# Performance work log

Hardware: AMD Instinct MI355X
Metric: run time of the kernel (lower is better)

## Reference

```python
import jax, jax.numpy as jnp
from jax import lax
import numpy as np

H = 128          # hidden_dim
VOCAB = 200000   # word_dim
L = 32           # words per node
NUM_LEAVES = 2048
NUM_PARENTS = 2047
MAXC = 4         # max child slots in a tree row
NCLASS = 4


def setup_inputs() -> dict:
    key = jax.random.key(0)
    ks = jax.random.split(key, 16)
    N = NUM_LEAVES + NUM_PARENTS
    x_word = jax.random.uniform(ks[0], (N, L), dtype=jnp.float32)
    x_index = jax.random.randint(ks[1], (N, L), 0, VOCAB)
    # caterpillar tree: parent idx has one leaf child and the previous parent
    idx = np.arange(NUM_PARENTS)
    tree = np.full((NUM_PARENTS, MAXC), -1, dtype=np.int32)
    tree[:, 0] = idx
    tree[:, 1] = np.where(idx > 0, NUM_LEAVES + idx - 1, NUM_LEAVES - 1)
    tree = jnp.asarray(tree)
    y = jax.random.uniform(ks[2], (NCLASS,), dtype=jnp.float32)
    def init(k, shp):
        return 0.1 * jax.random.normal(k, shp, dtype=jnp.float32)
    return dict(
        x_word=x_word, x_index=x_index, tree=tree, y=y,
        E_bu=init(ks[3], (H, VOCAB)),
        WQ=init(ks[4], (H, H)), WK=init(ks[5], (H, H)), WV=init(ks[6], (H, H)),
        W_z=init(ks[7], (H, H)), U_z=init(ks[8], (H, H)), b_z=jnp.zeros((H,), jnp.float32),
        W_r=init(ks[9], (H, H)), U_r=init(ks[10], (H, H)), b_r=jnp.zeros((H,), jnp.float32),
        W_h=init(ks[11], (H, H)), U_h=init(ks[12], (H, H)), b_h=jnp.zeros((H,), jnp.float32),
        W_out=init(ks[13], (NCLASS, H)), b_out=jnp.zeros((NCLASS,), jnp.float32),
    )


def _forward(x_word, y, E_bu, WQ, WK, WV, W_z, U_z, b_z, W_r, U_r, b_r,
             W_h, U_h, b_h, W_out, b_out, x_index, tree):
    Hd = E_bu.shape[0]
    # parent_xe for every node: weighted sum of embedding columns  [N, H]
    emb = E_bu.T[x_index]                        # [N, L, H] gather
    xe = jnp.einsum('nlh,nl->nh', emb, x_word)
    n_parents = tree.shape[0]
    n_leaves = x_word.shape[0] - n_parents

    def cell(xe_i, h_tilde):
        # W.mul(v).sum(dim=1) == W @ v in the torch code
        z = jax.nn.sigmoid(W_z @ xe_i + U_z @ h_tilde + b_z)
        r = jax.nn.sigmoid(W_r @ xe_i + U_r @ h_tilde + b_r)
        c = jnp.tanh(W_h @ xe_i + U_h @ (h_tilde * r) + b_h)
        return z * h_tilde + (1.0 - z) * c

    # leaves: child_h == 0  =>  h_tilde == 0 (vectorized over all leaves)
    xe_leaf = xe[:n_leaves]
    z_l = jax.nn.sigmoid(xe_leaf @ W_z.T + b_z)
    c_l = jnp.tanh(xe_leaf @ W_h.T + b_h)
    leaf_h = (1.0 - z_l) * c_l

    node_h0 = jnp.zeros((x_word.shape[0], Hd), xe.dtype).at[:n_leaves].set(leaf_h)
    scale = 1.0 / jnp.sqrt(jnp.asarray(Hd, xe.dtype))

    def step(node_h, inp):
        xe_p, row, i = inp
        mask = row >= 0
        child_h = node_h[jnp.clip(row, 0)]                  # [MAXC, H]
        query = jax.nn.sigmoid(xe_p @ WQ)                   # sigmoid(xe @ WQ)
        keyv = child_h @ WK
        val = child_h @ WV
        scores = jnp.where(mask, (query * scale * keyv).sum(-1), -1e9)
        attn = jax.nn.softmax(scores)                       # over children
        h_tilde = attn @ val
        h = cell(xe_p, h_tilde)
        return node_h.at[i].set(h), h

    idxs = jnp.arange(n_parents) + n_leaves
    _, parent_hs = lax.scan(step, node_h0, (xe[n_leaves:], tree, idxs))
    root = parent_hs[-1]
    pred = jax.nn.softmax(W_out @ root + b_out)
    loss = jnp.sum((y - pred) ** 2)
    return pred, loss


def reference(x_word, x_index, tree, y, E_bu, WQ, WK, WV, W_z, U_z, b_z,
              W_r, U_r, b_r, W_h, U_h, b_h, W_out, b_out):
    return _forward(x_word, y, E_bu, WQ, WK, WV, W_z, U_z, b_z, W_r, U_r, b_r,
                    W_h, U_h, b_h, W_out, b_out, x_index, tree)
```

## Files before the change

kernel.cpp:

```cpp
#include <hip/hip_runtime.h>
#include <math.h>

#define HD 128
#define LW 32
#define VOCABN 200000
#define NLEAF 2048
#define NPAR 2047
#define NNODE 4095
#define MAXC 4
#define NCLASS 4
#define SCALE 0.08838834764831845f

#define OFF_XE   0
#define OFF_NODE 524160
#define OFF_W3   786304
#define OFF_WQ   851840
#define OFF_AZ   1113856
#define OFF_AR   1375872
#define OFF_AH   1637888
#define OFF_PREV 1899904
#define OFF_ES   2685952
#define OFF_HG   2688000
#define OFF_HTR  2688128
#define OFF_ET   2688256
#define WS_END   (OFF_ET + (size_t)VOCABN * HD)

#define BARL() asm volatile("s_waitcnt lgkmcnt(0)\n\ts_barrier" ::: "memory")
#define PIN4(v) asm volatile("" : "+v"((v).x), "+v"((v).y), "+v"((v).z), "+v"((v).w))
#define LD4(p, k) (*(const float4*)((p) + 4 * (k)))

typedef __attribute__((ext_vector_type(16))) float fx16;

#define CH(W, X, n4) { a0 += (W).x * (X)[4*(n4)+0] + (W).y * (X)[4*(n4)+1]; \
                       a1 += (W).z * (X)[4*(n4)+2] + (W).w * (X)[4*(n4)+3]; }

__global__ void k_xe(const float* __restrict__ xw, const int* __restrict__ xi,
                     const float* __restrict__ E, float* __restrict__ xe) {
    int n = blockIdx.x;
    int h = threadIdx.x;
    __shared__ int   sidx[LW];
    __shared__ float sw[LW];
    if (h < LW) { sidx[h] = xi[n * LW + h]; sw[h] = xw[n * LW + h]; }
    __syncthreads();
    float acc = 0.f;
#pragma unroll
    for (int l = 0; l < LW; ++l)
        acc += E[(size_t)h * VOCABN + sidx[l]] * sw[l];
    xe[(size_t)n * HD + h] = acc;
}

__global__ void k_transpose(const float* __restrict__ E, float* __restrict__ ET) {
    __shared__ float tile[32][33];
    int vb = blockIdx.x * 32, hb = blockIdx.y * 32;
    int tx = threadIdx.x, ty = threadIdx.y;
#pragma unroll
    for (int r = 0; r < 32; r += 8)
        tile[ty + r][tx] = E[(size_t)(hb + ty + r) * VOCABN + vb + tx];
    __syncthreads();
#pragma unroll
    for (int r = 0; r < 32; r += 8)
        ET[(size_t)(vb + ty + r) * HD + hb + tx] = tile[tx][ty + r];
}

__global__ void k_xe_t(const float* __restrict__ xw, const int* __restrict__ xi,
                       const float* __restrict__ ET, float* __restrict__ xe) {
    int n = blockIdx.x;
    int h = threadIdx.x;
    __shared__ int   sidx[LW];
    __shared__ float sw[LW];
    if (h < LW) { sidx[h] = xi[n * LW + h]; sw[h] = xw[n * LW + h]; }
    __syncthreads();
    float acc = 0.f;
#pragma unroll
    for (int l = 0; l < LW; ++l)
        acc += ET[(size_t)sidx[l] * HD + h] * sw[l];
    xe[(size_t)n * HD + h] = acc;
}

__global__ void k_leaf(const float* __restrict__ xe, const float* __restrict__ Wz,
                       const float* __restrict__ bz, const float* __restrict__ Wh,
                       const float* __restrict__ bh, float* __restrict__ node_h) {
    int n = blockIdx.x;
    int j = threadIdx.x;
    __shared__ float xl[HD];
    xl[j] = xe[(size_t)n * HD + j];
    __syncthreads();
    float az = bz[j], ah = bh[j];
    const float* wzr = Wz + (size_t)j * HD;
    const float* whr = Wh + (size_t)j * HD;
#pragma unroll 4
    for (int k = 0; k < HD; ++k) { az += wzr[k] * xl[k]; ah += whr[k] * xl[k]; }
    float z = 1.f / (1.f + expf(-az));
    float c = tanhf(ah);
    node_h[(size_t)n * HD + j] = (1.f - z) * c;
}

__global__ void k_fuse(const float* __restrict__ WV, const float* __restrict__ Uz,
                       const float* __restrict__ Ur, const float* __restrict__ Uh,
                       float* __restrict__ w3) {
    int r = blockIdx.x;
    int b = threadIdx.x;
    float v;
    if (r < 128) {
        v = WV[(size_t)b * HD + r];
    } else if (r < 384) {
        const float* u  = (r < 256 ? Uz + (size_t)(r - 128) * HD : Ur + (size_t)(r - 256) * HD);
        const float* wv = WV + (size_t)b * HD;
        float a = 0.f;
#pragma unroll 4
        for (int j = 0; j < HD; ++j) a += u[j] * wv[j];
        v = a;
    } else {
        v = Uh[(size_t)(r - 384) * HD + b];
    }
    w3[(size_t)r * HD + b] = v;
}

__global__ void k_ppre(const float* __restrict__ xe, const float* __restrict__ WQ,
                       const float* __restrict__ WK, const float* __restrict__ Wz,
                       const float* __restrict__ bz, const float* __restrict__ Wr,
                       const float* __restrict__ br, const float* __restrict__ Wh,
                       const float* __restrict__ bh, float* __restrict__ wq,
                       float* __restrict__ az, float* __restrict__ ar,
                       float* __restrict__ ah) {
    int i = blockIdx.x;
    int j = threadIdx.x;
    __shared__ float xl[HD], ql[HD];
    xl[j] = xe[(size_t)(NLEAF + i) * HD + j];
    __syncthreads();
    float q = 0.f;
#pragma unroll 4
    for (int h = 0; h < HD; ++h) q += xl[h] * WQ[(size_t)h * HD + j];
    ql[j] = 1.f / (1.f + expf(-q));
    __syncthreads();
    float w = 0.f;
#pragma unroll 4
    for (int k = 0; k < HD; ++k) w += WK[(size_t)j * HD + k] * ql[k];
    wq[(size_t)i * HD + j] = w;
    float vz = bz[j], vr = br[j], vh = bh[j];
#pragma unroll 4
    for (int k = 0; k < HD; ++k) {
        float xv = xl[k];
        vz += Wz[(size_t)j * HD + k] * xv;
        vr += Wr[(size_t)j * HD + k] * xv;
        vh += Wh[(size_t)j * HD + k] * xv;
    }
    az[(size_t)i * HD + j] = vz;
    ar[(size_t)i * HD + j] = vr;
    ah[(size_t)i * HD + j] = vh;
}

__global__ void k_chpre(const int* __restrict__ tree, const float* __restrict__ node_h,
                        const float* __restrict__ w3, const float* __restrict__ wq_all,
                        float* __restrict__ preVexp, float* __restrict__ expsum) {
    int i = blockIdx.x;
    int j = threadIdx.x;
    __shared__ float hl[HD];
    __shared__ float red[HD];
    float wqj = wq_all[(size_t)i * HD + j];
    float acc0 = 0.f, acc1 = 0.f, acc2 = 0.f, esum = 0.f;
    for (int c = 0; c < MAXC; ++c) {
        int child = tree[i * MAXC + c];
        if (child < 0 || child >= NLEAF) continue;
        __syncthreads();
        hl[j] = node_h[(size_t)child * HD + j];
        __syncthreads();
        red[j] = hl[j] * wqj;
        __syncthreads();
        for (int s = 64; s > 0; s >>= 1) {
            if (j < s) red[j] += red[j + s];
            __syncthreads();
        }
        float e = expf(red[0] * SCALE);
        float d0 = 0.f, d1 = 0.f, d2 = 0.f;
#pragma unroll 4
        for (int k = 0; k < HD; ++k) {
            float x = hl[k];
            d0 += w3[(size_t)j * HD + k] * x;
            d1 += w3[(size_t)(128 + j) * HD + k] * x;
            d2 += w3[(size_t)(256 + j) * HD + k] * x;
        }
        acc0 += e * d0; acc1 += e * d1; acc2 += e * d2; esum += e;
    }
    preVexp[(size_t)i * 384 + j]       = acc0;
    preVexp[(size_t)i * 384 + 128 + j] = acc1;
    preVexp[(size_t)i * 384 + 256 + j] = acc2;
    if (j == 0) expsum[i] = esum;
}

__global__ __launch_bounds__(768, 3) void k_seq(
    float* __restrict__ ws, const float* __restrict__ Wout,
    const float* __restrict__ bout, const float* __restrict__ y,
    float* __restrict__ out) {
    const float* w3      = ws + OFF_W3;
    const float* wq_all  = ws + OFF_WQ;
    const float* az_all  = ws + OFF_AZ;
    const float* ar_all  = ws + OFF_AR;
    const float* ah_all  = ws + OFF_AH;
    const float* preVexp = ws + OFF_PREV;
    const float* expsum  = ws + OFF_ES;
    float* h_glob   = ws + OFF_HG;
    float* htr_glob = ws + OFF_HTR;

    const int t   = threadIdx.x;
    const int l   = t & 63;
    const int w   = t >> 6;
    const int q   = w & 1;
    const int row = 64 * (w >> 1) + l;
    const int w8  = w & 7;
    const int kq  = w8 & 3;
    const int row3 = 64 * (w8 >> 2) + l;

    __shared__ float part1[768];
    __shared__ __align__(16) float part3[HD][4];
    __shared__ float sPart[2];
    __shared__ float h_lds[HD];
    __shared__ float outv[NCLASS];

    const float* wp = w3 + (size_t)row * HD + 64 * q;
    float4 A0 = LD4(wp, 0),  A1 = LD4(wp, 1),  A2 = LD4(wp, 2),  A3 = LD4(wp, 3),
           A4 = LD4(wp, 4),  A5 = LD4(wp, 5),  A6 = LD4(wp, 6),  A7 = LD4(wp, 7),
           A8 = LD4(wp, 8),  A9 = LD4(wp, 9),  A10 = LD4(wp, 10), A11 = LD4(wp, 11),
           A12 = LD4(wp, 12), A13 = LD4(wp, 13), A14 = LD4(wp, 14), A15 = LD4(wp, 15);
    const float* wp3 = w3 + (size_t)(384 + row3) * HD + 32 * kq;
    float4 B0 = LD4(wp3, 0), B1 = LD4(wp3, 1), B2 = LD4(wp3, 2), B3 = LD4(wp3, 3),
           B4 = LD4(wp3, 4), B5 = LD4(wp3, 5), B6 = LD4(wp3, 6), B7 = LD4(wp3, 7);
    PIN4(A0); PIN4(A1); PIN4(A2); PIN4(A3); PIN4(A4); PIN4(A5); PIN4(A6); PIN4(A7);
    PIN4(A8); PIN4(A9); PIN4(A10); PIN4(A11); PIN4(A12); PIN4(A13); PIN4(A14); PIN4(A15);
    PIN4(B0); PIN4(B1); PIN4(B2); PIN4(B3); PIN4(B4); PIN4(B5); PIN4(B6); PIN4(B7);

    const float* xp1 = h_glob + __builtin_amdgcn_readfirstlane(64 * q);
    const float* xp3 = htr_glob + __builtin_amdgcn_readfirstlane(32 * kq);

    float pv0 = 0.f, pv1 = 0.f, pv2 = 0.f, paz = 0.f, par = 0.f, pah = 0.f,
          pwq = 0.f, pes = 0.f;
    if (t < HD) {
        pv0 = preVexp[t];       pv1 = preVexp[128 + t]; pv2 = preVexp[256 + t];
        paz = az_all[t];        par = ar_all[t];        pah = ah_all[t];
        pwq = wq_all[(size_t)HD + t];
        pes = expsum[0];
        h_glob[t] = 0.f;
    }
    if (t < 2) sPart[t] = (t == 0) ? -1e30f : 0.f;
    asm volatile("s_waitcnt vmcnt(0)" ::: "memory");
    __syncthreads();

    float zreg = 0.f, htreg = 0.f, hfin = 0.f;

    for (int i = 0; i < NPAR; ++i) {
        const int inext = (i + 1 < NPAR) ? i + 1 : NPAR - 1;
        const int in2   = (i + 2 < NPAR) ? i + 2 : NPAR - 1;

        {
            fx16 x0, x1, x2, x3;
            asm volatile(
                "s_dcache_inv\n\t"
                "s_load_dwordx16 %0, %4, 0x0\n\t"
                "s_load_dwordx16 %1, %4, 0x40\n\t"
                "s_load_dwordx16 %2, %4, 0x80\n\t"
                "s_load_dwordx16 %3, %4, 0xC0\n\t"
                "s_waitcnt lgkmcnt(0)"
                : "=s"(x0), "=s"(x1), "=s"(x2), "=s"(x3)
                : "s"(xp1));
            float a0 = 0.f, a1 = 0.f;
            CH(A0, x0, 0)  CH(A1, x0, 1)  CH(A2, x0, 2)  CH(A3, x0, 3)
            CH(A4, x1, 0)  CH(A5, x1, 1)  CH(A6, x1, 2)  CH(A7, x1, 3)
            CH(A8, x2, 0)  CH(A9, x2, 1)  CH(A10, x2, 2) CH(A11, x2, 3)
            CH(A12, x3, 0) CH(A13, x3, 1) CH(A14, x3, 2) CH(A15, x3, 3)
            part1[q * 384 + row] = a0 + a1;
        }
        BARL();

        if (t < HD) {
            float vdot = part1[t]       + part1[384 + t];
            float zdot = part1[128 + t] + part1[384 + 128 + t];
            float rdot = part1[256 + t] + part1[384 + 256 + t];
            float sc   = sPart[0] + sPart[1];
            float e    = expf(sc);
            float inv  = 1.f / (pes + e);
            float htv  = (pv0 + e * vdot) * inv;
            float z    = 1.f / (1.f + expf(-(paz + (pv1 + e * zdot) * inv)));
            float rr   = 1.f / (1.f + expf(-(par + (pv2 + e * rdot) * inv)));
            htr_glob[t] = htv * rr;
            zreg = z; htreg = htv;
            asm volatile("s_waitcnt vmcnt(0)" ::: "memory");
        }
        BARL();

        if (w < 8) {
            fx16 x0, x1;
            asm volatile(
                "s_dcache_inv\n\t"
                "s_load_dwordx16 %0, %2, 0x0\n\t"
                "s_load_dwordx16 %1, %2, 0x40\n\t"
                "s_waitcnt lgkmcnt(0)"
                : "=s"(x0), "=s"(x1)
                : "s"(xp3));
            float a0 = 0.f, a1 = 0.f;
            CH(B0, x0, 0) CH(B1, x0, 1) CH(B2, x0, 2) CH(B3, x0, 3)
            CH(B4, x1, 0) CH(B5, x1, 1) CH(B6, x1, 2) CH(B7, x1, 3)
            part3[row3][kq] = a0 + a1;
        }
        BARL();

        if (t < HD) {
            float4 p3 = *(const float4*)part3[t];
            float u   = (p3.x + p3.y) + (p3.z + p3.w);
            float c   = tanhf(pah + u);
            float hv  = zreg * htreg + (1.f - zreg) * c;
            hfin = hv;
            h_glob[t] = hv;
            pv0 = preVexp[(size_t)inext * 384 + t];
            pv1 = preVexp[(size_t)inext * 384 + 128 + t];
            pv2 = preVexp[(size_t)inext * 384 + 256 + t];
            paz = az_all[(size_t)inext * HD + t];
            par = ar_all[(size_t)inext * HD + t];
            pah = ah_all[(size_t)inext * HD + t];
            pes = expsum[inext];
            float prod = hv * pwq;
#pragma unroll
            for (int o = 32; o > 0; o >>= 1) prod += __shfl_down(prod, o, 64);
            if (l == 0) sPart[t >> 6] = prod * SCALE;
            pwq = wq_all[(size_t)in2 * HD + t];
            asm volatile("s_waitcnt vmcnt(0)" ::: "memory");
        }
        BARL();
    }

    if (t < HD) h_lds[t] = hfin;
    __syncthreads();
    if (t < NCLASS) {
        float acc = bout[t];
#pragma unroll 4
        for (int k = 0; k < HD; ++k) acc += Wout[(size_t)t * HD + k] * h_lds[k];
        outv[t] = acc;
    }
    __syncthreads();
    if (t == 0) {
        float m  = fmaxf(fmaxf(outv[0], outv[1]), fmaxf(outv[2], outv[3]));
        float e0 = expf(outv[0] - m), e1 = expf(outv[1] - m);
        float e2 = expf(outv[2] - m), e3 = expf(outv[3] - m);
        float inv = 1.f / (e0 + e1 + e2 + e3);
        float p0 = e0 * inv, p1 = e1 * inv, p2 = e2 * inv, p3 = e3 * inv;
        out[0] = p0; out[1] = p1; out[2] = p2; out[3] = p3;
        float d0 = y[0] - p0, d1 = y[1] - p1, d2 = y[2] - p2, d3 = y[3] - p3;
        out[4] = d0 * d0 + d1 * d1 + d2 * d2 + d3 * d3;
    }
}

extern "C" void kernel_launch(void* const* d_in, const int* in_sizes, int n_in,
                              void* d_out, int out_size, void* d_ws, size_t ws_size,
                              hipStream_t stream) {
    const float* x_word  = (const float*)d_in[0];
    const int*   x_index = (const int*)d_in[1];
    const int*   tree    = (const int*)d_in[2];
    const float* y       = (const float*)d_in[3];
    const float* E_bu    = (const float*)d_in[4];
    const float* WQ      = (const float*)d_in[5];
    const float* WK      = (const float*)d_in[6];
    const float* WV      = (const float*)d_in[7];
    const float* W_z     = (const float*)d_in[8];
    const float* U_z     = (const float*)d_in[9];
    const float* b_z     = (const float*)d_in[10];
    const float* W_r     = (const float*)d_in[11];
    const float* U_r     = (const float*)d_in[12];
    const float* b_r     = (const float*)d_in[13];
    const float* W_h     = (const float*)d_in[14];
    const float* U_h     = (const float*)d_in[15];
    const float* b_h     = (const float*)d_in[16];
    const float* W_out   = (const float*)d_in[17];
    const float* b_out   = (const float*)d_in[18];

    float* ws      = (float*)d_ws;
    float* xe      = ws + OFF_XE;
    float* node_h  = ws + OFF_NODE;
    float* w3      = ws + OFF_W3;
    float* wq      = ws + OFF_WQ;
    float* az      = ws + OFF_AZ;
    float* ar      = ws + OFF_AR;
    float* ah      = ws + OFF_AH;
    float* preVexp = ws + OFF_PREV;
    float* expsum  = ws + OFF_ES;
    float* ET      = ws + OFF_ET;

    bool use_transpose = ws_size >= WS_END * sizeof(float);

    if (use_transpose) {
        dim3 tg(VOCABN / 32, HD / 32), tb(32, 8);
        k_transpose<<<tg, tb, 0, stream>>>(E_bu, ET);
        k_xe_t<<<NNODE, HD, 0, stream>>>(x_word, x_index, ET, xe);
    } else {
        k_xe<<<NNODE, HD, 0, stream>>>(x_word, x_index, E_bu, xe);
    }
    k_leaf<<<NLEAF, HD, 0, stream>>>(xe, W_z, b_z, W_h, b_h, node_h);
    k_fuse<<<512, HD, 0, stream>>>(WV, U_z, U_r, U_h, w3);
    k_ppre<<<NPAR, HD, 0, stream>>>(xe, WQ, WK, W_z, b_z, W_r, b_r, W_h, b_h,
                                    wq, az, ar, ah);
    k_chpre<<<NPAR, HD, 0, stream>>>(tree, node_h, w3, wq, preVexp, expsum);
    k_seq<<<1, 768, 0, stream>>>(ws, W_out, b_out, y, (float*)d_out);
}
```

Before: 4.415 ms.

## Split sequential GRU phases onto dedicated waves in 1024-thread block

The single-block sequential kernel grows from 768 to 1024 threads. Waves 0-11 hold the V/Z/R recurrent weights and waves 12-15 hold the U_h weights, each as 64 registers, so no wave keeps two weight sets and the second matvec is split two ways instead of four. The prefetch of the next step's precomputed terms moves from the last phase into the second phase so it overlaps the U_h matvec. More waves per block raise register pressure under the 4-waves-per-EU limit and add extra waves at every barrier.

```diff
diff --git a/kernel.cpp b/kernel.cpp
--- a/kernel.cpp
+++ b/kernel.cpp
@@ -33,6 +33,10 @@
 
 #define CH(W, X, n4) { a0 += (W).x * (X)[4*(n4)+0] + (W).y * (X)[4*(n4)+1]; \
                        a1 += (W).z * (X)[4*(n4)+2] + (W).w * (X)[4*(n4)+3]; }
+
+#define PIN_ALL() do { PIN4(A0); PIN4(A1); PIN4(A2); PIN4(A3); \
+    PIN4(A4); PIN4(A5); PIN4(A6); PIN4(A7); PIN4(A8); PIN4(A9); \
+    PIN4(A10); PIN4(A11); PIN4(A12); PIN4(A13); PIN4(A14); PIN4(A15); } while (0)
 
 __global__ void k_xe(const float* __restrict__ xw, const int* __restrict__ xi,
                      const float* __restrict__ E, float* __restrict__ xe) {
@@ -188,70 +192,63 @@
     if (j == 0) expsum[i] = esum;
 }
 
-__global__ __launch_bounds__(768, 3) void k_seq(
-    float* __restrict__ ws, const float* __restrict__ Wout,
-    const float* __restrict__ bout, const float* __restrict__ y,
-    float* __restrict__ out) {
-    const float* w3      = ws + OFF_W3;
-    const float* wq_all  = ws + OFF_WQ;
-    const float* az_all  = ws + OFF_AZ;
-    const float* ar_all  = ws + OFF_AR;
-    const float* ah_all  = ws + OFF_AH;
-    const float* preVexp = ws + OFF_PREV;
-    const float* expsum  = ws + OFF_ES;
-    float* h_glob   = ws + OFF_HG;
-    float* htr_glob = ws + OFF_HTR;
-
-    const int t   = threadIdx.x;
-    const int l   = t & 63;
-    const int w   = t >> 6;
-    const int q   = w & 1;
-    const int row = 64 * (w >> 1) + l;
-    const int w8  = w & 7;
-    const int kq  = w8 & 3;
-    const int row3 = 64 * (w8 >> 2) + l;
+__global__ __launch_bounds__(1024)
+__attribute__((amdgpu_waves_per_eu(4, 4)))
+void k_seq(float* __restrict__ ws, const float* __restrict__ Wout,
+           const float* __restrict__ bout, const float* __restrict__ y,
+           float* __restrict__ out) {
+    const int t  = threadIdx.x;
+    const int l  = t & 63;
+    const int w  = t >> 6;
+    const bool isP1 = (w < 12);
+    const int q1   = w & 1;
+    const int row1 = 64 * (w >> 1) + l;
+    const int w12  = w - 12;
+    const int q3   = w12 & 1;
+    const int row3 = 64 * (w12 >> 1) + l;
 
     __shared__ float part1[768];
-    __shared__ __align__(16) float part3[HD][4];
+    __shared__ float part3[256];
     __shared__ float sPart[2];
     __shared__ float h_lds[HD];
     __shared__ float outv[NCLASS];
 
-    const float* wp = w3 + (size_t)row * HD + 64 * q;
+    const int woff = isP1 ? (row1 * HD + 64 * q1)
+                          : ((384 + row3) * HD + 64 * q3);
+    const float* wp = ws + OFF_W3 + woff;
     float4 A0 = LD4(wp, 0),  A1 = LD4(wp, 1),  A2 = LD4(wp, 2),  A3 = LD4(wp, 3),
            A4 = LD4(wp, 4),  A5 = LD4(wp, 5),  A6 = LD4(wp, 6),  A7 = LD4(wp, 7),
            A8 = LD4(wp, 8),  A9 = LD4(wp, 9),  A10 = LD4(wp, 10), A11 = LD4(wp, 11),
            A12 = LD4(wp, 12), A13 = LD4(wp, 13), A14 = LD4(wp, 14), A15 = LD4(wp, 15);
-    const float* wp3 = w3 + (size_t)(384 + row3) * HD + 32 * kq;
-    float4 B0 = LD4(wp3, 0), B1 = LD4(wp3, 1), B2 = LD4(wp3, 2), B3 = LD4(wp3, 3),
-           B4 = LD4(wp3, 4), B5 = LD4(wp3, 5), B6 = LD4(wp3, 6), B7 = LD4(wp3, 7);
-    PIN4(A0); PIN4(A1); PIN4(A2); PIN4(A3); PIN4(A4); PIN4(A5); PIN4(A6); PIN4(A7);
-    PIN4(A8); PIN4(A9); PIN4(A10); PIN4(A11); PIN4(A12); PIN4(A13); PIN4(A14); PIN4(A15);
-    PIN4(B0); PIN4(B1); PIN4(B2); PIN4(B3); PIN4(B4); PIN4(B5); PIN4(B6); PIN4(B7);
-
-    const float* xp1 = h_glob + __builtin_amdgcn_readfirstlane(64 * q);
-    const float* xp3 = htr_glob + __builtin_amdgcn_readfirstlane(32 * kq);
+    PIN_ALL();
+
+    const int xoff = isP1 ? (OFF_HG + 64 * q1) : (OFF_HTR + 64 * q3);
+    const float* xp = ws + __builtin_amdgcn_readfirstlane(xoff);
 
     float pv0 = 0.f, pv1 = 0.f, pv2 = 0.f, paz = 0.f, par = 0.f, pah = 0.f,
           pwq = 0.f, pes = 0.f;
     if (t < HD) {
-        pv0 = preVexp[t];       pv1 = preVexp[128 + t]; pv2 = preVexp[256 + t];
-        paz = az_all[t];        par = ar_all[t];        pah = ah_all[t];
-        pwq = wq_all[(size_t)HD + t];
-        pes = expsum[0];
-        h_glob[t] = 0.f;
+        pv0 = ws[OFF_PREV + t];       pv1 = ws[OFF_PREV + 128 + t];
+        pv2 = ws[OFF_PREV + 256 + t];
+        paz = ws[OFF_AZ + t];         par = ws[OFF_AR + t];
+        pah = ws[OFF_AH + t];
+        pwq = ws[OFF_WQ + HD + t];
+        pes = ws[OFF_ES];
+        ws[OFF_HG + t] = 0.f;
     }
     if (t < 2) sPart[t] = (t == 0) ? -1e30f : 0.f;
     asm volatile("s_waitcnt vmcnt(0)" ::: "memory");
     __syncthreads();
 
-    float zreg = 0.f, htreg = 0.f, hfin = 0.f;
+    float zreg = 0.f, htreg = 0.f, hfin = 0.f, cur_pah = 0.f, cur_pwq = 0.f;
 
     for (int i = 0; i < NPAR; ++i) {
         const int inext = (i + 1 < NPAR) ? i + 1 : NPAR - 1;
         const int in2   = (i + 2 < NPAR) ? i + 2 : NPAR - 1;
 
-        {
+        PIN_ALL();
+
+        if (isP1) {
             fx16 x0, x1, x2, x3;
             asm volatile(
                 "s_dcache_inv\n\t"
@@ -261,67 +258,71 @@
                 "s_load_dwordx16 %3, %4, 0xC0\n\t"
                 "s_waitcnt lgkmcnt(0)"
                 : "=s"(x0), "=s"(x1), "=s"(x2), "=s"(x3)
-                : "s"(xp1));
+                : "s"(xp));
             float a0 = 0.f, a1 = 0.f;
             CH(A0, x0, 0)  CH(A1, x0, 1)  CH(A2, x0, 2)  CH(A3, x0, 3)
             CH(A4, x1, 0)  CH(A5, x1, 1)  CH(A6, x1, 2)  CH(A7, x1, 3)
             CH(A8, x2, 0)  CH(A9, x2, 1)  CH(A10, x2, 2) CH(A11, x2, 3)
             CH(A12, x3, 0) CH(A13, x3, 1) CH(A14, x3, 2) CH(A15, x3, 3)
-            part1[q * 384 + row] = a0 + a1;
+            part1[q1 * 384 + row1] = a0 + a1;
         }
         BARL();
 
         if (t < HD) {
             float vdot = part1[t]       + part1[384 + t];
-            float zdot = part1[128 + t] + part1[384 + 128 + t];
-            float rdot = part1[256 + t] + part1[384 + 256 + t];
+            float zdot = part1[128 + t] + part1[512 + t];
+            float rdot = part1[256 + t] + part1[640 + t];
             float sc   = sPart[0] + sPart[1];
             float e    = expf(sc);
             float inv  = 1.f / (pes + e);
             float htv  = (pv0 + e * vdot) * inv;
             float z    = 1.f / (1.f + expf(-(paz + (pv1 + e * zdot) * inv)));
             float rr   = 1.f / (1.f + expf(-(par + (pv2 + e * rdot) * inv)));
-            htr_glob[t] = htv * rr;
+            ws[OFF_HTR + t] = htv * rr;
             zreg = z; htreg = htv;
             asm volatile("s_waitcnt vmcnt(0)" ::: "memory");
+            cur_pah = pah; cur_pwq = pwq;
+            pv0 = ws[OFF_PREV + inext * 384 + t];
+            pv1 = ws[OFF_PREV + inext * 384 + 128 + t];
+            pv2 = ws[OFF_PREV + inext * 384 + 256 + t];
+            paz = ws[OFF_AZ + inext * HD + t];
+            par = ws[OFF_AR + inext * HD + t];
+            pah = ws[OFF_AH + inext * HD + t];
+            pes = ws[OFF_ES + inext];
+            pwq = ws[OFF_WQ + in2 * HD + t];
         }
         BARL();
 
-        if (w < 8) {
-            fx16 x0, x1;
+        if (!isP1) {
+            fx16 x0, x1, x2, x3;
             asm volatile(
                 "s_dcache_inv\n\t"
-                "s_load_dwordx16 %0, %2, 0x0\n\t"
-                "s_load_dwordx16 %1, %2, 0x40\n\t"
+                "s_load_dwordx16 %0, %4, 0x0\n\t"
+                "s_load_dwordx16 %1, %4, 0x40\n\t"
+                "s_load_dwordx16 %2, %4, 0x80\n\t"
+                "s_load_dwordx16 %3, %4, 0xC0\n\t"
                 "s_waitcnt lgkmcnt(0)"
-                : "=s"(x0), "=s"(x1)
-                : "s"(xp3));
+                : "=s"(x0), "=s"(x1), "=s"(x2), "=s"(x3)
+                : "s"(xp));
             float a0 = 0.f, a1 = 0.f;
-            CH(B0, x0, 0) CH(B1, x0, 1) CH(B2, x0, 2) CH(B3, x0, 3)
-            CH(B4, x1, 0) CH(B5, x1, 1) CH(B6, x1, 2) CH(B7, x1, 3)
-            part3[row3][kq] = a0 + a1;
+            CH(A0, x0, 0)  CH(A1, x0, 1)  CH(A2, x0, 2)  CH(A3, x0, 3)
+            CH(A4, x1, 0)  CH(A5, x1, 1)  CH(A6, x1, 2)  CH(A7, x1, 3)
+            CH(A8, x2, 0)  CH(A9, x2, 1)  CH(A10, x2, 2) CH(A11, x2, 3)
+            CH(A12, x3, 0) CH(A13, x3, 1) CH(A14, x3, 2) CH(A15, x3, 3)
+            part3[q3 * 128 + row3] = a0 + a1;
         }
         BARL();
 
         if (t < HD) {
-            float4 p3 = *(const float4*)part3[t];
-            float u   = (p3.x + p3.y) + (p3.z + p3.w);
-            float c   = tanhf(pah + u);
-            float hv  = zreg * htreg + (1.f - zreg) * c;
+            float u  = part3[t] + part3[128 + t];
+            float c  = tanhf(cur_pah + u);
+            float hv = zreg * htreg + (1.f - zreg) * c;
             hfin = hv;
-            h_glob[t] = hv;
-            pv0 = preVexp[(size_t)inext * 384 + t];
-            pv1 = preVexp[(size_t)inext * 384 + 128 + t];
-            pv2 = preVexp[(size_t)inext * 384 + 256 + t];
-            paz = az_all[(size_t)inext * HD + t];
-            par = ar_all[(size_t)inext * HD + t];
-            pah = ah_all[(size_t)inext * HD + t];
-            pes = expsum[inext];
-            float prod = hv * pwq;
+            ws[OFF_HG + t] = hv;
+            float prod = hv * cur_pwq;
 #pragma unroll
             for (int o = 32; o > 0; o >>= 1) prod += __shfl_down(prod, o, 64);
-            if (l == 0) sPart[t >> 6] = prod * SCALE;
-            pwq = wq_all[(size_t)in2 * HD + t];
+            if (l == 0) sPart[w] = prod * SCALE;
             asm volatile("s_waitcnt vmcnt(0)" ::: "memory");
         }
         BARL();
@@ -397,5 +398,5 @@
     k_ppre<<<NPAR, HD, 0, stream>>>(xe, WQ, WK, W_z, b_z, W_r, b_r, W_h, b_h,
                                     wq, az, ar, ah);
     k_chpre<<<NPAR, HD, 0, stream>>>(tree, node_h, w3, wq, preVexp, expsum);
-    k_seq<<<1, 768, 0, stream>>>(ws, W_out, b_out, y, (float*)d_out);
-}
+    k_seq<<<1, 1024, 0, stream>>>(ws, W_out, b_out, y, (float*)d_out);
+}
```

After: 4.348 ms. Within noise of the previous version (-1.5%).
